# Kernel tuning notes

Hardware: AMD Instinct MI355X
Metric: run time of the kernel (lower is better)

Reference implementation:

```python
import jax, jax.numpy as jnp
import numpy as np

NEG_SLOPE = 0.2  # PyG GATv2Conv default negative_slope


def gatv2_layer(x, src, dst, n, Wl, bl, Wr, br, att, bias):
    """GATv2Conv with heads=1, concat=False, add aggregation.
    src -> dst edges; softmax normalized per destination node."""
    xl = x @ Wl + bl            # source-side transform  [N, C]
    xr = x @ Wr + br            # target-side transform  [N, C]
    m = jax.nn.leaky_relu(xl[src] + xr[dst], NEG_SLOPE)  # [E, C]
    e = m @ att                 # attention logits [E]
    emax = jax.ops.segment_max(e, dst, num_segments=n)
    emax = jnp.where(jnp.isfinite(emax), emax, 0.0)  # guard isolated nodes
    ex = jnp.exp(e - emax[dst])
    denom = jax.ops.segment_sum(ex, dst, num_segments=n)
    alpha = ex / denom[dst]     # ragged per-node softmax [E]
    out = jax.ops.segment_sum(alpha[:, None] * xl[src], dst, num_segments=n)
    return out + bias


def setup_inputs() -> dict:
    key = jax.random.key(0)
    ks = jax.random.split(key, 16)
    N, E = 50000, 800000
    C_in, C_h, C_out = 1, 256, 128

    def lin(k, fan_in, fan_out):
        s = (1.0 / np.sqrt(fan_in)).astype(np.float32) if isinstance(fan_in, np.ndarray) else 1.0 / np.sqrt(fan_in)
        return jax.random.normal(k, (fan_in, fan_out), dtype=jnp.float32) * s

    inp = {
        "x": jax.random.normal(ks[0], (N, C_in), dtype=jnp.float32),
        "edge_index": jax.random.randint(ks[1], (2, E), 0, N, dtype=jnp.int32),
        # layer 1 (1 -> 256)
        "Wl1": lin(ks[2], C_in, C_h),
        "bl1": jnp.zeros((C_h,), jnp.float32),
        "Wr1": lin(ks[3], C_in, C_h),
        "br1": jnp.zeros((C_h,), jnp.float32),
        "att1": jax.random.normal(ks[4], (C_h,), dtype=jnp.float32) / np.sqrt(C_h),
        "bias1": jnp.zeros((C_h,), jnp.float32),
        # PReLU (per-channel, init 0.25 like torch)
        "prelu_w": jnp.full((C_h,), 0.25, jnp.float32),
        # layer 2 (256 -> 128)
        "Wl2": lin(ks[5], C_h, C_out),
        "bl2": jnp.zeros((C_out,), jnp.float32),
        "Wr2": lin(ks[6], C_h, C_out),
        "br2": jnp.zeros((C_out,), jnp.float32),
        "att2": jax.random.normal(ks[7], (C_out,), dtype=jnp.float32) / np.sqrt(C_out),
        "bias2": jnp.zeros((C_out,), jnp.float32),
    }
    return inp


def reference(x, edge_index, Wl1, bl1, Wr1, br1, att1, bias1, prelu_w,
              Wl2, bl2, Wr2, br2, att2, bias2):
    n = x.shape[0]
    # PyG GATv2Conv default add_self_loops=True
    loops = jnp.arange(n, dtype=edge_index.dtype)
    src = jnp.concatenate([edge_index[0], loops])
    dst = jnp.concatenate([edge_index[1], loops])

    h = gatv2_layer(x, src, dst, n, Wl1, bl1, Wr1, br1, att1, bias1)
    h = jnp.where(h > 0, h, prelu_w * h)  # PReLU(hidden_channels)
    out = gatv2_layer(h, src, dst, n, Wl2, bl2, Wr2, br2, att2, bias2)
    return out
```

## Files before the change

kernel.cpp:

```cpp
#include <hip/hip_runtime.h>
#include <hip/hip_bf16.h>

#define SLOPE 0.2f

typedef __attribute__((ext_vector_type(8))) short short8;
typedef __attribute__((ext_vector_type(4))) float f32x4;

static __device__ __forceinline__ unsigned short f2bf(float f) {
  __hip_bfloat16 h = __float2bfloat16(f);
  return *reinterpret_cast<unsigned short*>(&h);
}

static __device__ __forceinline__ void packedReduce4(
    float q0, float q1, float q2, float q3,
    float& p0, float& p1, float& p2, float& p3) {
  int lane = threadIdx.x & 63;
  float u = (lane & 1) ? q1 : q0;
  float v = (lane & 1) ? q0 : q1;
  u += __shfl_xor(v, 1, 64);
  float w = (lane & 1) ? q3 : q2;
  float z = (lane & 1) ? q2 : q3;
  w += __shfl_xor(z, 1, 64);
  float a = (lane & 2) ? w : u;
  float b = (lane & 2) ? u : w;
  a += __shfl_xor(b, 2, 64);
  a += __shfl_xor(a, 4, 64);
  a += __shfl_xor(a, 8, 64);
  a += __shfl_xor(a, 16, 64);
  a += __shfl_xor(a, 32, 64);
  p0 = __shfl(a, 0, 64);
  p1 = __shfl(a, 1, 64);
  p2 = __shfl(a, 2, 64);
  p3 = __shfl(a, 3, 64);
}

__global__ void count_kernel(const int* __restrict__ ei, int E, int N,
                             int* __restrict__ deg, int* __restrict__ rank) {
  int t = blockIdx.x * blockDim.x + threadIdx.x;
  int Etot = E + N;
  int j0 = t * 8;
  if (j0 >= Etot) return;
  if (j0 + 8 <= E) {
    int4 a = *(const int4*)(ei + E + j0);
    int4 b = *(const int4*)(ei + E + j0 + 4);
    int4 ra, rb;
    ra.x = atomicAdd(&deg[a.x], 1); ra.y = atomicAdd(&deg[a.y], 1);
    ra.z = atomicAdd(&deg[a.z], 1); ra.w = atomicAdd(&deg[a.w], 1);
    rb.x = atomicAdd(&deg[b.x], 1); rb.y = atomicAdd(&deg[b.y], 1);
    rb.z = atomicAdd(&deg[b.z], 1); rb.w = atomicAdd(&deg[b.w], 1);
    *(int4*)(rank + j0) = ra;
    *(int4*)(rank + j0 + 4) = rb;
  } else {
#pragma unroll
    for (int i = 0; i < 8; ++i) {
      int j = j0 + i;
      if (j < Etot) {
        int d = (j < E) ? ei[E + j] : (j - E);
        rank[j] = atomicAdd(&deg[d], 1);
      }
    }
  }
}

__global__ __launch_bounds__(1024) void scan1_kernel(const int* __restrict__ deg, int N,
                                                     int* __restrict__ bsum) {
  __shared__ int ws[16];
  int i = blockIdx.x * 1024 + threadIdx.x;
  int v = (i < N) ? deg[i] : 0;
#pragma unroll
  for (int off = 32; off > 0; off >>= 1) v += __shfl_xor(v, off, 64);
  int wave = threadIdx.x >> 6;
  if ((threadIdx.x & 63) == 0) ws[wave] = v;
  __syncthreads();
  if (threadIdx.x == 0) {
    int s = 0;
#pragma unroll
    for (int k = 0; k < 16; ++k) s += ws[k];
    bsum[blockIdx.x] = s;
  }
}

__global__ __launch_bounds__(1024) void scan2_kernel(const int* __restrict__ bsum, int B,
                                                     int* __restrict__ boff) {
  __shared__ int s[1024];
  int tid = threadIdx.x;
  s[tid] = (tid < B) ? bsum[tid] : 0;
  __syncthreads();
  for (int off = 1; off < 1024; off <<= 1) {
    int t = (tid >= off) ? s[tid - off] : 0;
    __syncthreads();
    s[tid] += t;
    __syncthreads();
  }
  if (tid < B) boff[tid] = (tid == 0) ? 0 : s[tid - 1];
}

__global__ __launch_bounds__(1024) void scan3_kernel(const int* __restrict__ deg,
                                                     const int* __restrict__ boff, int N,
                                                     int* __restrict__ rowptr) {
  __shared__ int s[1024];
  int tid = threadIdx.x;
  int i = blockIdx.x * 1024 + tid;
  int v = (i < N) ? deg[i] : 0;
  s[tid] = v;
  __syncthreads();
  for (int off = 1; off < 1024; off <<= 1) {
    int t = (tid >= off) ? s[tid - off] : 0;
    __syncthreads();
    s[tid] += t;
    __syncthreads();
  }
  int base = boff[blockIdx.x];
  if (i < N) {
    rowptr[i] = base + s[tid] - v;
    if (i == N - 1) rowptr[N] = base + s[tid];
  }
}

__global__ void scatter_kernel(const int* __restrict__ ei, const int* __restrict__ rank,
                               const int* __restrict__ rowptr, int E, int N,
                               int* __restrict__ srcs) {
  int t = blockIdx.x * blockDim.x + threadIdx.x;
  int Etot = E + N;
  int j0 = t * 8;
  if (j0 >= Etot) return;
  if (j0 + 8 <= E) {
    int4 sa = *(const int4*)(ei + j0);
    int4 sb = *(const int4*)(ei + j0 + 4);
    int4 da = *(const int4*)(ei + E + j0);
    int4 db = *(const int4*)(ei + E + j0 + 4);
    int4 ra = *(const int4*)(rank + j0);
    int4 rb = *(const int4*)(rank + j0 + 4);
    srcs[rowptr[da.x] + ra.x] = sa.x;
    srcs[rowptr[da.y] + ra.y] = sa.y;
    srcs[rowptr[da.z] + ra.z] = sa.z;
    srcs[rowptr[da.w] + ra.w] = sa.w;
    srcs[rowptr[db.x] + rb.x] = sb.x;
    srcs[rowptr[db.y] + rb.y] = sb.y;
    srcs[rowptr[db.z] + rb.z] = sb.z;
    srcs[rowptr[db.w] + rb.w] = sb.w;
  } else {
#pragma unroll
    for (int i = 0; i < 8; ++i) {
      int j = j0 + i;
      if (j < Etot) {
        int s, d;
        if (j < E) { s = ei[j]; d = ei[E + j]; } else { s = j - E; d = j - E; }
        srcs[rowptr[d] + rank[j]] = s;
      }
    }
  }
}

__global__ __launch_bounds__(1024) void wcvt_kernel(
    const float* __restrict__ Wl2, const float* __restrict__ Wr2,
    __hip_bfloat16* __restrict__ Wt,
    const float* __restrict__ Wl1, const float* __restrict__ bl1,
    const float* __restrict__ Wr1, const float* __restrict__ br1,
    const float* __restrict__ att1, float* __restrict__ agd) {
  __shared__ float tile[32][33];
  int k0 = blockIdx.y * 32, c0 = blockIdx.x * 32;
  int tx = threadIdx.x & 31, ty = threadIdx.x >> 5;
  int k = k0 + ty, c = c0 + tx;
  float v = (c < 128) ? Wl2[(size_t)k * 128 + c] : Wr2[(size_t)k * 128 + (c - 128)];
  tile[ty][tx] = v;
  __syncthreads();
  Wt[(size_t)(c0 + ty) * 256 + k0 + tx] = __float2bfloat16(tile[tx][ty]);

  if (blockIdx.x == 0 && blockIdx.y == 0 && threadIdx.x < 64) {
    int lane = threadIdx.x;
    int cc = lane * 4;
    float4 wl = *(const float4*)(Wl1 + cc);
    float4 wr = *(const float4*)(Wr1 + cc);
    float4 ba = *(const float4*)(bl1 + cc);
    float4 bb = *(const float4*)(br1 + cc);
    float4 at = *(const float4*)(att1 + cc);
    float pa = at.x * wl.x + at.y * wl.y + at.z * wl.z + at.w * wl.w;
    float pg = at.x * wr.x + at.y * wr.y + at.z * wr.z + at.w * wr.w;
    float pd = at.x * (ba.x + bb.x) + at.y * (ba.y + bb.y) +
               at.z * (ba.z + bb.z) + at.w * (ba.w + bb.w);
#pragma unroll
    for (int off = 32; off > 0; off >>= 1) {
      pa += __shfl_xor(pa, off, 64);
      pg += __shfl_xor(pg, off, 64);
      pd += __shfl_xor(pd, off, 64);
    }
    if (lane == 0) { agd[0] = pa; agd[1] = pg; agd[2] = pd; }
  }
}

__global__ __launch_bounds__(256) void l1_fused_kernel(
    const float* __restrict__ x, const int* __restrict__ srcs,
    const int* __restrict__ rowptr, int N,
    const float* __restrict__ Wl1, const float* __restrict__ bl1,
    const float* __restrict__ Wr1, const float* __restrict__ br1,
    const float* __restrict__ att1, const float* __restrict__ agd,
    float* __restrict__ S1) {
  int wid = (blockIdx.x * blockDim.x + threadIdx.x) >> 6;
  int lane = threadIdx.x & 63;
  if (wid >= N) return;
  int c0 = lane * 4;
  float4 wl = *(const float4*)(Wl1 + c0);
  float4 wr = *(const float4*)(Wr1 + c0);
  float4 ba = *(const float4*)(bl1 + c0);
  float4 bb = *(const float4*)(br1 + c0);
  float4 at = *(const float4*)(att1 + c0);
  float xd = x[wid];
  float cc0 = fmaf(xd, wr.x, ba.x + bb.x);
  float cc1 = fmaf(xd, wr.y, ba.y + bb.y);
  float cc2 = fmaf(xd, wr.z, ba.z + bb.z);
  float cc3 = fmaf(xd, wr.w, ba.w + bb.w);
  float a40 = 0.4f * at.x, a41 = 0.4f * at.y, a42 = 0.4f * at.z, a43 = 0.4f * at.w;
  float alpha = agd[0], gamma = agd[1], delta = agd[2];
  float beta = fmaf(xd, gamma, delta);
  float al6 = 0.6f * alpha, be6 = 0.6f * beta;

  int base = rowptr[wid], end = rowptr[wid + 1];
  float m = -INFINITY, S = 0.f, vs = 0.f;
  for (int k0 = base; k0 < end; k0 += 4) {
    int k1 = min(k0 + 1, end - 1);
    int k2 = min(k0 + 2, end - 1);
    int k3 = min(k0 + 3, end - 1);
    float xs0 = x[srcs[k0]];
    float xs1 = x[srcs[k1]];
    float xs2 = x[srcs[k2]];
    float xs3 = x[srcs[k3]];

    float q0, q1, q2, q3;
    {
      float z0, z1, z2, z3;
#define L1ABS(xs, q)                                                      \
      z0 = fmaf(xs, wl.x, cc0); z1 = fmaf(xs, wl.y, cc1);                 \
      z2 = fmaf(xs, wl.z, cc2); z3 = fmaf(xs, wl.w, cc3);                 \
      q = fmaf(fabsf(z0), a40, fmaf(fabsf(z1), a41,                       \
            fmaf(fabsf(z2), a42, fabsf(z3) * a43)));
      L1ABS(xs0, q0) L1ABS(xs1, q1) L1ABS(xs2, q2) L1ABS(xs3, q3)
#undef L1ABS
    }
    float p0, p1, p2, p3;
    packedReduce4(q0, q1, q2, q3, p0, p1, p2, p3);
    p0 += fmaf(xs0, al6, be6);
    p1 += fmaf(xs1, al6, be6);
    p2 += fmaf(xs2, al6, be6);
    p3 += fmaf(xs3, al6, be6);
    if (k0 + 1 >= end) p1 = -INFINITY;
    if (k0 + 2 >= end) p2 = -INFINITY;
    if (k0 + 3 >= end) p3 = -INFINITY;

    float pmax = fmaxf(fmaxf(p0, p1), fmaxf(p2, p3));
    if (pmax > m) {
      float sc = __expf(m - pmax);
      S *= sc; vs *= sc;
      m = pmax;
    }
    float w0 = __expf(p0 - m), w1 = __expf(p1 - m);
    float w2 = __expf(p2 - m), w3 = __expf(p3 - m);
    S += (w0 + w1) + (w2 + w3);
    vs += fmaf(w0, xs0, fmaf(w1, xs1, fmaf(w2, xs2, w3 * xs3)));
  }
  if (lane == 0) S1[wid] = vs / S;
}

__global__ __launch_bounds__(512) void l2_transform_mfma(
    const float* __restrict__ S1,
    const float* __restrict__ Wl1, const float* __restrict__ bl1,
    const float* __restrict__ bias1, const float* __restrict__ prelu_w,
    const __hip_bfloat16* __restrict__ Wt,
    const float* __restrict__ bl2, const float* __restrict__ br2,
    int N, unsigned short* __restrict__ xl2b, unsigned short* __restrict__ xr2b) {
  int w = threadIdx.x >> 6;
  int lane = threadIdx.x & 63;
  int l15 = lane & 15, lk = lane >> 4;
  int rbase = blockIdx.x * 128 + (w & 1) * 64;
  int cbase = (w >> 1) * 64;

  float s1v[4];
#pragma unroll
  for (int mt = 0; mt < 4; ++mt) {
    int r = rbase + mt * 16 + l15;
    s1v[mt] = (r < N) ? S1[r] : 0.f;
  }

  f32x4 acc[4][4] = {};

#pragma unroll
  for (int ks = 0; ks < 8; ++ks) {
    int k0 = ks * 32 + lk * 8;
    float4 wl1a = *(const float4*)(Wl1 + k0);
    float4 wl1b = *(const float4*)(Wl1 + k0 + 4);
    float4 b1a  = *(const float4*)(bl1 + k0);
    float4 b1b  = *(const float4*)(bl1 + k0 + 4);
    float4 z1a  = *(const float4*)(bias1 + k0);
    float4 z1b  = *(const float4*)(bias1 + k0 + 4);
    float4 pwa  = *(const float4*)(prelu_w + k0);
    float4 pwb  = *(const float4*)(prelu_w + k0 + 4);
    float wv[8] = {wl1a.x, wl1a.y, wl1a.z, wl1a.w, wl1b.x, wl1b.y, wl1b.z, wl1b.w};
    float cv[8] = {b1a.x + z1a.x, b1a.y + z1a.y, b1a.z + z1a.z, b1a.w + z1a.w,
                   b1b.x + z1b.x, b1b.y + z1b.y, b1b.z + z1b.z, b1b.w + z1b.w};
    float pv[8] = {pwa.x, pwa.y, pwa.z, pwa.w, pwb.x, pwb.y, pwb.z, pwb.w};

    short8 afrag[4];
#pragma unroll
    for (int mt = 0; mt < 4; ++mt) {
      short8 a;
#pragma unroll
      for (int j = 0; j < 8; ++j) {
        float t = fmaf(wv[j], s1v[mt], cv[j]);
        t = (t > 0.f) ? t : pv[j] * t;
        a[j] = (short)f2bf(t);
      }
      afrag[mt] = a;
    }

    short8 bfrag[4];
#pragma unroll
    for (int nt = 0; nt < 4; ++nt) {
      int col = cbase + nt * 16 + l15;
      bfrag[nt] = *(const short8*)(Wt + (size_t)col * 256 + k0);
    }

#pragma unroll
    for (int mt = 0; mt < 4; ++mt)
#pragma unroll
      for (int nt = 0; nt < 4; ++nt)
        acc[mt][nt] = __builtin_amdgcn_mfma_f32_16x16x32_bf16(afrag[mt], bfrag[nt],
                                                              acc[mt][nt], 0, 0, 0);
  }

#pragma unroll
  for (int mt = 0; mt < 4; ++mt) {
#pragma unroll
    for (int nt = 0; nt < 4; ++nt) {
      int col = cbase + nt * 16 + l15;
      float bias;
      unsigned short* dst;
      int cc;
      if (col < 128) { bias = bl2[col]; dst = xl2b; cc = col; }
      else           { bias = br2[col - 128]; dst = xr2b; cc = col - 128; }
#pragma unroll
      for (int r = 0; r < 4; ++r) {
        int row = rbase + mt * 16 + lk * 4 + r;
        if (row < N) dst[(size_t)row * 128 + cc] = f2bf(acc[mt][nt][r] + bias);
      }
    }
  }
}

__global__ __launch_bounds__(256) void l2_fused_kernel(
    const unsigned short* __restrict__ xl2b, const unsigned short* __restrict__ xr2b,
    const int* __restrict__ srcs, const int* __restrict__ rowptr,
    const float* __restrict__ att2, const float* __restrict__ bias2,
    int N, float* __restrict__ out) {
  int wid = (blockIdx.x * blockDim.x + threadIdx.x) >> 6;
  int lane = threadIdx.x & 63;
  if (wid >= N) return;
  unsigned c0 = (unsigned)(lane * 2);
  float2 at = *(const float2*)(att2 + c0);
  unsigned qd = *(const unsigned*)(xr2b + (((unsigned)wid << 7) + c0));
  float drx = __uint_as_float(qd << 16);
  float dry = __uint_as_float(qd & 0xffff0000u);
  int base = rowptr[wid], end = rowptr[wid + 1];
  float m = -INFINITY, S = 0.f, a0 = 0.f, a1 = 0.f;
  for (int k0 = base; k0 < end; k0 += 4) {
    int k1 = min(k0 + 1, end - 1);
    int k2 = min(k0 + 2, end - 1);
    int k3 = min(k0 + 3, end - 1);
    unsigned s0 = (unsigned)srcs[k0], s1 = (unsigned)srcs[k1];
    unsigned s2 = (unsigned)srcs[k2], s3 = (unsigned)srcs[k3];
    unsigned q0 = *(const unsigned*)(xl2b + ((s0 << 7) + c0));
    unsigned q1 = *(const unsigned*)(xl2b + ((s1 << 7) + c0));
    unsigned q2 = *(const unsigned*)(xl2b + ((s2 << 7) + c0));
    unsigned q3 = *(const unsigned*)(xl2b + ((s3 << 7) + c0));
    float r0x = __uint_as_float(q0 << 16), r0y = __uint_as_float(q0 & 0xffff0000u);
    float r1x = __uint_as_float(q1 << 16), r1y = __uint_as_float(q1 & 0xffff0000u);
    float r2x = __uint_as_float(q2 << 16), r2y = __uint_as_float(q2 & 0xffff0000u);
    float r3x = __uint_as_float(q3 << 16), r3y = __uint_as_float(q3 & 0xffff0000u);

    float e0, e1, e2, e3;
    {
      float v0, v1;
#define L2DOT(rx, ry, q)                                        \
      v0 = rx + drx; v0 = fmaxf(v0, SLOPE * v0);                \
      v1 = ry + dry; v1 = fmaxf(v1, SLOPE * v1);                \
      q = fmaf(v0, at.x, v1 * at.y);
      L2DOT(r0x, r0y, e0) L2DOT(r1x, r1y, e1) L2DOT(r2x, r2y, e2) L2DOT(r3x, r3y, e3)
#undef L2DOT
    }
    float p0, p1, p2, p3;
    packedReduce4(e0, e1, e2, e3, p0, p1, p2, p3);
    if (k0 + 1 >= end) p1 = -INFINITY;
    if (k0 + 2 >= end) p2 = -INFINITY;
    if (k0 + 3 >= end) p3 = -INFINITY;

    float pmax = fmaxf(fmaxf(p0, p1), fmaxf(p2, p3));
    if (pmax > m) {
      float sc = __expf(m - pmax);
      S *= sc; a0 *= sc; a1 *= sc;
      m = pmax;
    }
    float w0 = __expf(p0 - m), w1 = __expf(p1 - m);
    float w2 = __expf(p2 - m), w3 = __expf(p3 - m);
    S += (w0 + w1) + (w2 + w3);
    a0 += fmaf(w0, r0x, fmaf(w1, r1x, fmaf(w2, r2x, w3 * r3x)));
    a1 += fmaf(w0, r0y, fmaf(w1, r1y, fmaf(w2, r2y, w3 * r3y)));
  }
  float inv = 1.f / S;
  float2 bz = *(const float2*)(bias2 + c0);
  float2 res;
  res.x = fmaf(a0, inv, bz.x);
  res.y = fmaf(a1, inv, bz.y);
  *(float2*)(out + (((unsigned)wid << 7) + c0)) = res;
}

extern "C" void kernel_launch(void* const* d_in, const int* in_sizes, int n_in,
                              void* d_out, int out_size, void* d_ws, size_t ws_size,
                              hipStream_t stream) {
  const float* x      = (const float*)d_in[0];
  const int*   ei     = (const int*)d_in[1];
  const float* Wl1    = (const float*)d_in[2];
  const float* bl1    = (const float*)d_in[3];
  const float* Wr1    = (const float*)d_in[4];
  const float* br1    = (const float*)d_in[5];
  const float* att1   = (const float*)d_in[6];
  const float* bias1  = (const float*)d_in[7];
  const float* prelu  = (const float*)d_in[8];
  const float* Wl2    = (const float*)d_in[9];
  const float* bl2    = (const float*)d_in[10];
  const float* Wr2    = (const float*)d_in[11];
  const float* br2    = (const float*)d_in[12];
  const float* att2   = (const float*)d_in[13];
  const float* bias2  = (const float*)d_in[14];
  float* out = (float*)d_out;

  int N = in_sizes[0];
  int E = in_sizes[1] / 2;
  int Etot = E + N;

  char* ws = (char*)d_ws;
  size_t off = 0;
  auto alloc = [&](size_t bytes) -> void* {
    void* p = ws + off;
    off = (off + bytes + 255) & ~(size_t)255;
    return p;
  };
  float* S1     = (float*)alloc((size_t)N * 4);
  unsigned short* xl2b = (unsigned short*)alloc((size_t)N * 128 * 2);
  unsigned short* xr2b = (unsigned short*)alloc((size_t)N * 128 * 2);
  int*   deg    = (int*)alloc((size_t)N * 4);
  int*   rowptr = (int*)alloc((size_t)(N + 1) * 4);
  int*   rank   = (int*)alloc((size_t)Etot * 4);
  int*   srcs   = (int*)alloc((size_t)Etot * 4);
  int*   bsum   = (int*)alloc((size_t)1024 * 4);
  int*   boff   = (int*)alloc((size_t)1024 * 4);
  float* agd    = (float*)alloc((size_t)16 * 4);
  __hip_bfloat16* Wt = (__hip_bfloat16*)alloc((size_t)256 * 256 * 2);
  (void)ws_size; (void)n_in; (void)out_size;

  hipMemsetAsync(deg, 0, (size_t)N * 4, stream);

  int B = (N + 1023) / 1024;
  int g8 = (Etot + 8 * 256 - 1) / (8 * 256);
  count_kernel<<<g8, 256, 0, stream>>>(ei, E, N, deg, rank);
  scan1_kernel<<<B, 1024, 0, stream>>>(deg, N, bsum);
  scan2_kernel<<<1, 1024, 0, stream>>>(bsum, B, boff);
  scan3_kernel<<<B, 1024, 0, stream>>>(deg, boff, N, rowptr);
  scatter_kernel<<<g8, 256, 0, stream>>>(ei, rank, rowptr, E, N, srcs);

  wcvt_kernel<<<dim3(8, 8), 1024, 0, stream>>>(Wl2, Wr2, Wt,
                                               Wl1, bl1, Wr1, br1, att1, agd);

  l1_fused_kernel<<<(N + 3) / 4, 256, 0, stream>>>(x, srcs, rowptr, N,
                                                   Wl1, bl1, Wr1, br1, att1, agd, S1);
  l2_transform_mfma<<<(N + 127) / 128, 512, 0, stream>>>(S1, Wl1, bl1, bias1, prelu,
                                                         Wt, bl2, br2, N, xl2b, xr2b);
  l2_fused_kernel<<<(N + 3) / 4, 256, 0, stream>>>(xl2b, xr2b, srcs, rowptr,
                                                   att2, bias2, N, out);
}
```

Baseline: 281.6 us.

## Split each wave into two half-waves processing edges, place self-loops in scan

```diff
diff --git a/kernel.cpp b/kernel.cpp
--- a/kernel.cpp
+++ b/kernel.cpp
@@ -1,7 +1,7 @@
 #include <hip/hip_runtime.h>
 #include <hip/hip_bf16.h>
 
-#define SLOPE 0.2f
+#define L2E 1.44269504088896f
 
 typedef __attribute__((ext_vector_type(8))) short short8;
 typedef __attribute__((ext_vector_type(4))) float f32x4;
@@ -11,10 +11,9 @@
   return *reinterpret_cast<unsigned short*>(&h);
 }
 
-static __device__ __forceinline__ void packedReduce4(
-    float q0, float q1, float q2, float q3,
+static __device__ __forceinline__ void halfReduce4(
+    float q0, float q1, float q2, float q3, int lane,
     float& p0, float& p1, float& p2, float& p3) {
-  int lane = threadIdx.x & 63;
   float u = (lane & 1) ? q1 : q0;
   float v = (lane & 1) ? q0 : q1;
   u += __shfl_xor(v, 1, 64);
@@ -27,19 +26,18 @@
   a += __shfl_xor(a, 4, 64);
   a += __shfl_xor(a, 8, 64);
   a += __shfl_xor(a, 16, 64);
-  a += __shfl_xor(a, 32, 64);
-  p0 = __shfl(a, 0, 64);
-  p1 = __shfl(a, 1, 64);
-  p2 = __shfl(a, 2, 64);
-  p3 = __shfl(a, 3, 64);
-}
-
-__global__ void count_kernel(const int* __restrict__ ei, int E, int N,
+  int h32 = lane & 32;
+  p0 = __shfl(a, h32, 64);
+  p1 = __shfl(a, h32 + 1, 64);
+  p2 = __shfl(a, h32 + 2, 64);
+  p3 = __shfl(a, h32 + 3, 64);
+}
+
+__global__ void count_kernel(const int* __restrict__ ei, int E,
                              int* __restrict__ deg, int* __restrict__ rank) {
   int t = blockIdx.x * blockDim.x + threadIdx.x;
-  int Etot = E + N;
   int j0 = t * 8;
-  if (j0 >= Etot) return;
+  if (j0 >= E) return;
   if (j0 + 8 <= E) {
     int4 a = *(const int4*)(ei + E + j0);
     int4 b = *(const int4*)(ei + E + j0 + 4);
@@ -54,10 +52,7 @@
 #pragma unroll
     for (int i = 0; i < 8; ++i) {
       int j = j0 + i;
-      if (j < Etot) {
-        int d = (j < E) ? ei[E + j] : (j - E);
-        rank[j] = atomicAdd(&deg[d], 1);
-      }
+      if (j < E) rank[j] = atomicAdd(&deg[ei[E + j]], 1);
     }
   }
 }
@@ -66,7 +61,7 @@
                                                      int* __restrict__ bsum) {
   __shared__ int ws[16];
   int i = blockIdx.x * 1024 + threadIdx.x;
-  int v = (i < N) ? deg[i] : 0;
+  int v = (i < N) ? deg[i] + 1 : 0;
 #pragma unroll
   for (int off = 32; off > 0; off >>= 1) v += __shfl_xor(v, off, 64);
   int wave = threadIdx.x >> 6;
@@ -97,11 +92,12 @@
 
 __global__ __launch_bounds__(1024) void scan3_kernel(const int* __restrict__ deg,
                                                      const int* __restrict__ boff, int N,
-                                                     int* __restrict__ rowptr) {
+                                                     int* __restrict__ rowptr,
+                                                     int* __restrict__ srcs) {
   __shared__ int s[1024];
   int tid = threadIdx.x;
   int i = blockIdx.x * 1024 + tid;
-  int v = (i < N) ? deg[i] : 0;
+  int v = (i < N) ? deg[i] + 1 : 0;
   s[tid] = v;
   __syncthreads();
   for (int off = 1; off < 1024; off <<= 1) {
@@ -112,18 +108,19 @@
   }
   int base = boff[blockIdx.x];
   if (i < N) {
-    rowptr[i] = base + s[tid] - v;
-    if (i == N - 1) rowptr[N] = base + s[tid];
+    int incl = base + s[tid];
+    rowptr[i] = incl - v;
+    srcs[incl - 1] = i;
+    if (i == N - 1) rowptr[N] = incl;
   }
 }
 
 __global__ void scatter_kernel(const int* __restrict__ ei, const int* __restrict__ rank,
-                               const int* __restrict__ rowptr, int E, int N,
+                               const int* __restrict__ rowptr, int E,
                                int* __restrict__ srcs) {
   int t = blockIdx.x * blockDim.x + threadIdx.x;
-  int Etot = E + N;
   int j0 = t * 8;
-  if (j0 >= Etot) return;
+  if (j0 >= E) return;
   if (j0 + 8 <= E) {
     int4 sa = *(const int4*)(ei + j0);
     int4 sb = *(const int4*)(ei + j0 + 4);
@@ -143,11 +140,7 @@
 #pragma unroll
     for (int i = 0; i < 8; ++i) {
       int j = j0 + i;
-      if (j < Etot) {
-        int s, d;
-        if (j < E) { s = ei[j]; d = ei[E + j]; } else { s = j - E; d = j - E; }
-        srcs[rowptr[d] + rank[j]] = s;
-      }
+      if (j < E) srcs[rowptr[ei[E + j]] + rank[j]] = ei[j];
     }
   }
 }
@@ -199,66 +192,77 @@
   int wid = (blockIdx.x * blockDim.x + threadIdx.x) >> 6;
   int lane = threadIdx.x & 63;
   if (wid >= N) return;
-  int c0 = lane * 4;
-  float4 wl = *(const float4*)(Wl1 + c0);
-  float4 wr = *(const float4*)(Wr1 + c0);
-  float4 ba = *(const float4*)(bl1 + c0);
-  float4 bb = *(const float4*)(br1 + c0);
-  float4 at = *(const float4*)(att1 + c0);
+  int h4 = (lane >> 5) << 2;
+  int sl = lane & 31;
+  int c0 = sl * 8;
+
+  float4 wv0 = *(const float4*)(Wl1 + c0), wv1 = *(const float4*)(Wl1 + c0 + 4);
+  float4 rv0 = *(const float4*)(Wr1 + c0), rv1 = *(const float4*)(Wr1 + c0 + 4);
+  float4 p10 = *(const float4*)(bl1 + c0), p11 = *(const float4*)(bl1 + c0 + 4);
+  float4 p20 = *(const float4*)(br1 + c0), p21 = *(const float4*)(br1 + c0 + 4);
+  float4 av0 = *(const float4*)(att1 + c0), av1 = *(const float4*)(att1 + c0 + 4);
   float xd = x[wid];
-  float cc0 = fmaf(xd, wr.x, ba.x + bb.x);
-  float cc1 = fmaf(xd, wr.y, ba.y + bb.y);
-  float cc2 = fmaf(xd, wr.z, ba.z + bb.z);
-  float cc3 = fmaf(xd, wr.w, ba.w + bb.w);
-  float a40 = 0.4f * at.x, a41 = 0.4f * at.y, a42 = 0.4f * at.z, a43 = 0.4f * at.w;
+  float wl[8] = {wv0.x, wv0.y, wv0.z, wv0.w, wv1.x, wv1.y, wv1.z, wv1.w};
+  float wr[8] = {rv0.x, rv0.y, rv0.z, rv0.w, rv1.x, rv1.y, rv1.z, rv1.w};
+  float bsum[8] = {p10.x + p20.x, p10.y + p20.y, p10.z + p20.z, p10.w + p20.w,
+                   p11.x + p21.x, p11.y + p21.y, p11.z + p21.z, p11.w + p21.w};
+  float atv[8] = {av0.x, av0.y, av0.z, av0.w, av1.x, av1.y, av1.z, av1.w};
+  float cc[8], a4[8];
+#pragma unroll
+  for (int j = 0; j < 8; ++j) {
+    cc[j] = fmaf(xd, wr[j], bsum[j]);
+    a4[j] = 0.4f * L2E * atv[j];
+  }
   float alpha = agd[0], gamma = agd[1], delta = agd[2];
   float beta = fmaf(xd, gamma, delta);
-  float al6 = 0.6f * alpha, be6 = 0.6f * beta;
+  float al6 = 0.6f * L2E * alpha, be6 = 0.6f * L2E * beta;
 
   int base = rowptr[wid], end = rowptr[wid + 1];
-  float m = -INFINITY, S = 0.f, vs = 0.f;
-  for (int k0 = base; k0 < end; k0 += 4) {
-    int k1 = min(k0 + 1, end - 1);
-    int k2 = min(k0 + 2, end - 1);
-    int k3 = min(k0 + 3, end - 1);
-    float xs0 = x[srcs[k0]];
-    float xs1 = x[srcs[k1]];
-    float xs2 = x[srcs[k2]];
-    float xs3 = x[srcs[k3]];
-
-    float q0, q1, q2, q3;
-    {
-      float z0, z1, z2, z3;
-#define L1ABS(xs, q)                                                      \
-      z0 = fmaf(xs, wl.x, cc0); z1 = fmaf(xs, wl.y, cc1);                 \
-      z2 = fmaf(xs, wl.z, cc2); z3 = fmaf(xs, wl.w, cc3);                 \
-      q = fmaf(fabsf(z0), a40, fmaf(fabsf(z1), a41,                       \
-            fmaf(fabsf(z2), a42, fabsf(z3) * a43)));
-      L1ABS(xs0, q0) L1ABS(xs1, q1) L1ABS(xs2, q2) L1ABS(xs3, q3)
-#undef L1ABS
+  int e1 = end - 1;
+  float m = -1e30f, S = 0.f, vs = 0.f;
+  for (int kb = base; kb < end; kb += 8) {
+    int k0 = kb + h4;
+    int kc0 = min(k0, e1), kc1 = min(k0 + 1, e1);
+    int kc2 = min(k0 + 2, e1), kc3 = min(k0 + 3, e1);
+    float xs0 = x[srcs[kc0]], xs1 = x[srcs[kc1]];
+    float xs2 = x[srcs[kc2]], xs3 = x[srcs[kc3]];
+
+    float q0 = 0.f, q1 = 0.f, q2 = 0.f, q3 = 0.f;
+#pragma unroll
+    for (int j = 0; j < 8; ++j) {
+      float z0 = fmaf(xs0, wl[j], cc[j]); q0 = fmaf(fabsf(z0), a4[j], q0);
+      float z1 = fmaf(xs1, wl[j], cc[j]); q1 = fmaf(fabsf(z1), a4[j], q1);
+      float z2 = fmaf(xs2, wl[j], cc[j]); q2 = fmaf(fabsf(z2), a4[j], q2);
+      float z3 = fmaf(xs3, wl[j], cc[j]); q3 = fmaf(fabsf(z3), a4[j], q3);
     }
     float p0, p1, p2, p3;
-    packedReduce4(q0, q1, q2, q3, p0, p1, p2, p3);
+    halfReduce4(q0, q1, q2, q3, lane, p0, p1, p2, p3);
     p0 += fmaf(xs0, al6, be6);
     p1 += fmaf(xs1, al6, be6);
     p2 += fmaf(xs2, al6, be6);
     p3 += fmaf(xs3, al6, be6);
-    if (k0 + 1 >= end) p1 = -INFINITY;
-    if (k0 + 2 >= end) p2 = -INFINITY;
-    if (k0 + 3 >= end) p3 = -INFINITY;
+    if (k0     > e1) p0 = -INFINITY;
+    if (k0 + 1 > e1) p1 = -INFINITY;
+    if (k0 + 2 > e1) p2 = -INFINITY;
+    if (k0 + 3 > e1) p3 = -INFINITY;
 
     float pmax = fmaxf(fmaxf(p0, p1), fmaxf(p2, p3));
     if (pmax > m) {
-      float sc = __expf(m - pmax);
-      S *= sc; vs *= sc;
-      m = pmax;
-    }
-    float w0 = __expf(p0 - m), w1 = __expf(p1 - m);
-    float w2 = __expf(p2 - m), w3 = __expf(p3 - m);
+      float sc = exp2f(m - pmax);
+      S *= sc; vs *= sc; m = pmax;
+    }
+    float w0 = exp2f(p0 - m), w1 = exp2f(p1 - m);
+    float w2 = exp2f(p2 - m), w3 = exp2f(p3 - m);
     S += (w0 + w1) + (w2 + w3);
     vs += fmaf(w0, xs0, fmaf(w1, xs1, fmaf(w2, xs2, w3 * xs3)));
   }
-  if (lane == 0) S1[wid] = vs / S;
+  float mo = __shfl_xor(m, 32, 64);
+  float mm = fmaxf(m, mo);
+  float sc = exp2f(m - mm);
+  float Sh = S * sc, vh = vs * sc;
+  Sh += __shfl_xor(Sh, 32, 64);
+  vh += __shfl_xor(vh, 32, 64);
+  if (lane == 0) S1[wid] = vh / Sh;
 }
 
 __global__ __launch_bounds__(512) void l2_transform_mfma(
@@ -354,62 +358,93 @@
   int wid = (blockIdx.x * blockDim.x + threadIdx.x) >> 6;
   int lane = threadIdx.x & 63;
   if (wid >= N) return;
-  unsigned c0 = (unsigned)(lane * 2);
-  float2 at = *(const float2*)(att2 + c0);
-  unsigned qd = *(const unsigned*)(xr2b + (((unsigned)wid << 7) + c0));
-  float drx = __uint_as_float(qd << 16);
-  float dry = __uint_as_float(qd & 0xffff0000u);
+  int h4 = (lane >> 5) << 2;
+  int sl = lane & 31;
+  unsigned c0 = (unsigned)(sl * 4);
+
+  float4 at = *(const float4*)(att2 + c0);
+  float t60 = 0.6f * L2E * at.x, t61 = 0.6f * L2E * at.y;
+  float t62 = 0.6f * L2E * at.z, t63 = 0.6f * L2E * at.w;
+  float t40 = 0.4f * L2E * at.x, t41 = 0.4f * L2E * at.y;
+  float t42 = 0.4f * L2E * at.z, t43 = 0.4f * L2E * at.w;
+  uint2 du = *(const uint2*)(xr2b + ((unsigned)wid * 128u) + c0);
+  float d0 = __uint_as_float(du.x << 16), d1 = __uint_as_float(du.x & 0xffff0000u);
+  float d2 = __uint_as_float(du.y << 16), d3 = __uint_as_float(du.y & 0xffff0000u);
+
   int base = rowptr[wid], end = rowptr[wid + 1];
-  float m = -INFINITY, S = 0.f, a0 = 0.f, a1 = 0.f;
-  for (int k0 = base; k0 < end; k0 += 4) {
-    int k1 = min(k0 + 1, end - 1);
-    int k2 = min(k0 + 2, end - 1);
-    int k3 = min(k0 + 3, end - 1);
-    unsigned s0 = (unsigned)srcs[k0], s1 = (unsigned)srcs[k1];
-    unsigned s2 = (unsigned)srcs[k2], s3 = (unsigned)srcs[k3];
-    unsigned q0 = *(const unsigned*)(xl2b + ((s0 << 7) + c0));
-    unsigned q1 = *(const unsigned*)(xl2b + ((s1 << 7) + c0));
-    unsigned q2 = *(const unsigned*)(xl2b + ((s2 << 7) + c0));
-    unsigned q3 = *(const unsigned*)(xl2b + ((s3 << 7) + c0));
-    float r0x = __uint_as_float(q0 << 16), r0y = __uint_as_float(q0 & 0xffff0000u);
-    float r1x = __uint_as_float(q1 << 16), r1y = __uint_as_float(q1 & 0xffff0000u);
-    float r2x = __uint_as_float(q2 << 16), r2y = __uint_as_float(q2 & 0xffff0000u);
-    float r3x = __uint_as_float(q3 << 16), r3y = __uint_as_float(q3 & 0xffff0000u);
-
-    float e0, e1, e2, e3;
-    {
-      float v0, v1;
-#define L2DOT(rx, ry, q)                                        \
-      v0 = rx + drx; v0 = fmaxf(v0, SLOPE * v0);                \
-      v1 = ry + dry; v1 = fmaxf(v1, SLOPE * v1);                \
-      q = fmaf(v0, at.x, v1 * at.y);
-      L2DOT(r0x, r0y, e0) L2DOT(r1x, r1y, e1) L2DOT(r2x, r2y, e2) L2DOT(r3x, r3y, e3)
-#undef L2DOT
-    }
+  int e1 = end - 1;
+  float m = -1e30f, S = 0.f;
+  float a0 = 0.f, a1 = 0.f, a2 = 0.f, a3 = 0.f;
+  for (int kb = base; kb < end; kb += 8) {
+    int k0 = kb + h4;
+    int kc0 = min(k0, e1), kc1 = min(k0 + 1, e1);
+    int kc2 = min(k0 + 2, e1), kc3 = min(k0 + 3, e1);
+    unsigned s0 = (unsigned)srcs[kc0], s1 = (unsigned)srcs[kc1];
+    unsigned s2 = (unsigned)srcs[kc2], s3 = (unsigned)srcs[kc3];
+    uint2 u0 = *(const uint2*)(xl2b + (s0 << 7) + c0);
+    uint2 u1 = *(const uint2*)(xl2b + (s1 << 7) + c0);
+    uint2 u2 = *(const uint2*)(xl2b + (s2 << 7) + c0);
+    uint2 u3 = *(const uint2*)(xl2b + (s3 << 7) + c0);
+    float r00 = __uint_as_float(u0.x << 16), r01 = __uint_as_float(u0.x & 0xffff0000u);
+    float r02 = __uint_as_float(u0.y << 16), r03 = __uint_as_float(u0.y & 0xffff0000u);
+    float r10 = __uint_as_float(u1.x << 16), r11 = __uint_as_float(u1.x & 0xffff0000u);
+    float r12 = __uint_as_float(u1.y << 16), r13 = __uint_as_float(u1.y & 0xffff0000u);
+    float r20 = __uint_as_float(u2.x << 16), r21 = __uint_as_float(u2.x & 0xffff0000u);
+    float r22 = __uint_as_float(u2.y << 16), r23 = __uint_as_float(u2.y & 0xffff0000u);
+    float r30 = __uint_as_float(u3.x << 16), r31 = __uint_as_float(u3.x & 0xffff0000u);
+    float r32 = __uint_as_float(u3.y << 16), r33 = __uint_as_float(u3.y & 0xffff0000u);
+
+    float q0, q1, q2, q3;
+#define L2Q(rA, rB, rC, rD, q) {                                          \
+      float v0 = rA + d0, v1 = rB + d1, v2 = rC + d2, v3 = rD + d3;       \
+      q = fmaf(t60, v0, fmaf(t40, fabsf(v0),                              \
+          fmaf(t61, v1, fmaf(t41, fabsf(v1),                              \
+          fmaf(t62, v2, fmaf(t42, fabsf(v2),                              \
+          fmaf(t63, v3, t43 * fabsf(v3)))))))); }
+    L2Q(r00, r01, r02, r03, q0)
+    L2Q(r10, r11, r12, r13, q1)
+    L2Q(r20, r21, r22, r23, q2)
+    L2Q(r30, r31, r32, r33, q3)
+#undef L2Q
+
     float p0, p1, p2, p3;
-    packedReduce4(e0, e1, e2, e3, p0, p1, p2, p3);
-    if (k0 + 1 >= end) p1 = -INFINITY;
-    if (k0 + 2 >= end) p2 = -INFINITY;
-    if (k0 + 3 >= end) p3 = -INFINITY;
+    halfReduce4(q0, q1, q2, q3, lane, p0, p1, p2, p3);
+    if (k0     > e1) p0 = -INFINITY;
+    if (k0 + 1 > e1) p1 = -INFINITY;
+    if (k0 + 2 > e1) p2 = -INFINITY;
+    if (k0 + 3 > e1) p3 = -INFINITY;
 
     float pmax = fmaxf(fmaxf(p0, p1), fmaxf(p2, p3));
     if (pmax > m) {
-      float sc = __expf(m - pmax);
-      S *= sc; a0 *= sc; a1 *= sc;
+      float sc = exp2f(m - pmax);
+      S *= sc; a0 *= sc; a1 *= sc; a2 *= sc; a3 *= sc;
       m = pmax;
     }
-    float w0 = __expf(p0 - m), w1 = __expf(p1 - m);
-    float w2 = __expf(p2 - m), w3 = __expf(p3 - m);
+    float w0 = exp2f(p0 - m), w1 = exp2f(p1 - m);
+    float w2 = exp2f(p2 - m), w3 = exp2f(p3 - m);
     S += (w0 + w1) + (w2 + w3);
-    a0 += fmaf(w0, r0x, fmaf(w1, r1x, fmaf(w2, r2x, w3 * r3x)));
-    a1 += fmaf(w0, r0y, fmaf(w1, r1y, fmaf(w2, r2y, w3 * r3y)));
-  }
-  float inv = 1.f / S;
-  float2 bz = *(const float2*)(bias2 + c0);
-  float2 res;
-  res.x = fmaf(a0, inv, bz.x);
-  res.y = fmaf(a1, inv, bz.y);
-  *(float2*)(out + (((unsigned)wid << 7) + c0)) = res;
+    a0 += fmaf(w0, r00, fmaf(w1, r10, fmaf(w2, r20, w3 * r30)));
+    a1 += fmaf(w0, r01, fmaf(w1, r11, fmaf(w2, r21, w3 * r31)));
+    a2 += fmaf(w0, r02, fmaf(w1, r12, fmaf(w2, r22, w3 * r32)));
+    a3 += fmaf(w0, r03, fmaf(w1, r13, fmaf(w2, r23, w3 * r33)));
+  }
+  float mo = __shfl_xor(m, 32, 64);
+  float mm = fmaxf(m, mo);
+  float sc = exp2f(m - mm);
+  float Sh = S * sc;
+  float b0 = a0 * sc, b1 = a1 * sc, b2 = a2 * sc, b3 = a3 * sc;
+  Sh += __shfl_xor(Sh, 32, 64);
+  b0 += __shfl_xor(b0, 32, 64);
+  b1 += __shfl_xor(b1, 32, 64);
+  b2 += __shfl_xor(b2, 32, 64);
+  b3 += __shfl_xor(b3, 32, 64);
+  if (lane < 32) {
+    float inv = 1.f / Sh;
+    float4 bz = *(const float4*)(bias2 + c0);
+    float4 res = make_float4(fmaf(b0, inv, bz.x), fmaf(b1, inv, bz.y),
+                             fmaf(b2, inv, bz.z), fmaf(b3, inv, bz.w));
+    *(float4*)(out + ((unsigned)wid * 128u) + c0) = res;
+  }
 }
 
 extern "C" void kernel_launch(void* const* d_in, const int* in_sizes, int n_in,
@@ -448,7 +483,7 @@
   unsigned short* xr2b = (unsigned short*)alloc((size_t)N * 128 * 2);
   int*   deg    = (int*)alloc((size_t)N * 4);
   int*   rowptr = (int*)alloc((size_t)(N + 1) * 4);
-  int*   rank   = (int*)alloc((size_t)Etot * 4);
+  int*   rank   = (int*)alloc((size_t)E * 4);
   int*   srcs   = (int*)alloc((size_t)Etot * 4);
   int*   bsum   = (int*)alloc((size_t)1024 * 4);
   int*   boff   = (int*)alloc((size_t)1024 * 4);
@@ -459,12 +494,12 @@
   hipMemsetAsync(deg, 0, (size_t)N * 4, stream);
 
   int B = (N + 1023) / 1024;
-  int g8 = (Etot + 8 * 256 - 1) / (8 * 256);
-  count_kernel<<<g8, 256, 0, stream>>>(ei, E, N, deg, rank);
+  int gE8 = (E + 8 * 256 - 1) / (8 * 256);
+  count_kernel<<<gE8, 256, 0, stream>>>(ei, E, deg, rank);
   scan1_kernel<<<B, 1024, 0, stream>>>(deg, N, bsum);
   scan2_kernel<<<1, 1024, 0, stream>>>(bsum, B, boff);
-  scan3_kernel<<<B, 1024, 0, stream>>>(deg, boff, N, rowptr);
-  scatter_kernel<<<g8, 256, 0, stream>>>(ei, rank, rowptr, E, N, srcs);
+  scan3_kernel<<<B, 1024, 0, stream>>>(deg, boff, N, rowptr, srcs);
+  scatter_kernel<<<gE8, 256, 0, stream>>>(ei, rank, rowptr, E, srcs);
 
   wcvt_kernel<<<dim3(8, 8), 1024, 0, stream>>>(Wl2, Wr2, Wt,
                                                Wl1, bl1, Wr1, br1, att1, agd);
```

Result: faster. 270.5 us (-3.9%).
